# Performance work log

Measured on AMD Instinct MI355X. Metric: run time of the kernel, lower is better.

The kernel has to match this reference:

```python
import jax, jax.numpy as jnp
import numpy as np

N_NODES = 50000
N_EDGES = 640000
D_IN = 128
D_OUT = 128


def setup_inputs() -> dict:
    key = jax.random.key(0)
    k1, k2, k3, k4 = jax.random.split(key, 4)
    x = jax.random.normal(k1, (N_NODES, D_IN), dtype=jnp.float32)
    edge_index = jax.random.randint(k2, (2, N_EDGES), 0, N_NODES, dtype=jnp.int64)
    weight = jax.random.uniform(k3, (1,), dtype=jnp.float32)
    temperature = jnp.ones((1,), dtype=jnp.float32)
    W = jax.random.normal(k4, (D_IN, D_OUT), dtype=jnp.float32) * (1.0 / np.sqrt(D_IN))
    b = jnp.zeros((D_OUT,), dtype=jnp.float32)
    return {"x": x, "edge_index": edge_index, "weight": weight,
            "temperature": temperature, "W": W, "b": b}


def _gcn_conv(x, edge_index, W, b):
    N = x.shape[0]
    src, dst = edge_index[0], edge_index[1]
    loop = jnp.arange(N, dtype=edge_index.dtype)
    s = jnp.concatenate([src, loop])  # self-loops appended
    d = jnp.concatenate([dst, loop])
    deg = jax.ops.segment_sum(jnp.ones(s.shape[0], dtype=x.dtype), d, num_segments=N)
    dinv = jnp.where(deg > 0, deg ** -0.5, 0.0)
    norm = dinv[s] * dinv[d]  # [E+N]
    h = x @ W                 # linear transform first (PyG GCNConv)
    msg = h[s] * norm[:, None]
    out = jax.ops.segment_sum(msg, d, num_segments=N)
    return out + b


def _gradient_entropy(x, edge_index, temperature):
    # Boltzmann distribution over per-node Dirichlet energies;
    # entropy gradient w.r.t. node features (computed with autodiff).
    N = x.shape[0]
    src, dst = edge_index[0], edge_index[1]

    def entropy(z):
        diff = z[src] - z[dst]                                  # [E, D]
        E = jax.ops.segment_sum(jnp.sum(diff * diff, axis=-1), dst, num_segments=N)
        logp = jax.nn.log_softmax(-E / temperature[0])
        p = jnp.exp(logp)
        return -jnp.sum(p * logp)

    return jax.grad(entropy)(x)


def reference(x, edge_index, weight, temperature, W, b):
    h = _gcn_conv(x, edge_index, W, b)
    g = jax.lax.stop_gradient(_gradient_entropy(h, edge_index, temperature))
    return h + weight * g
```

## Files before the change

kernel.cpp:

```cpp
#include <hip/hip_runtime.h>

#define N_NODES 50000
#define N_EDGES 640000

#define OFF_HTMPB    0
#define OFF_OBF      3200000
#define OFF_DEG      6400000
#define OFF_ROWSTART 6450000
#define OFF_CURSOR   6500016
#define OFF_DINV     6550016
#define OFF_E        6600016
#define OFF_SCAL     6650016
#define OFF_BLKSUM   6650020
#define OFF_ESRC     6650276

typedef __attribute__((ext_vector_type(4))) short bf16x4;
typedef __attribute__((ext_vector_type(8))) short bf16x8;
typedef __attribute__((ext_vector_type(4))) float f32x4;

__device__ __forceinline__ unsigned short f2bf(float f) {
    unsigned u = __float_as_uint(f);
    unsigned r = u + 0x7fffu + ((u >> 16) & 1u);
    return (unsigned short)(r >> 16);
}
__device__ __forceinline__ float bflo(unsigned u) { return __uint_as_float(u << 16); }
__device__ __forceinline__ float bfhi(unsigned u) { return __uint_as_float(u & 0xffff0000u); }

__global__ __launch_bounds__(256) void k_init(float* ws) {
    int i = blockIdx.x * 256 + threadIdx.x;
    if (i < N_NODES) ((int*)(ws + OFF_DEG))[i] = 0;
    if (i == 0) {
        ((int*)(ws + OFF_SCAL))[0] = 0x7F7FFFFF;
        ws[OFF_SCAL + 1] = 0.f;
        ws[OFF_SCAL + 2] = 0.f;
    }
}

__global__ __launch_bounds__(256) void k_deg(const int* __restrict__ dst, int* __restrict__ deg) {
    int e = blockIdx.x * 256 + threadIdx.x;
    atomicAdd(&deg[dst[e]], 1);
}

__global__ __launch_bounds__(256) void k_gemm(const float* __restrict__ x,
                                              const float* __restrict__ W,
                                              unsigned short* __restrict__ htmpb) {
    __shared__ unsigned short xs[128 * 132];
    __shared__ unsigned short wt[128 * 132];
    int tid = threadIdx.x;
    int r0 = blockIdx.x * 128;

    #pragma unroll
    for (int i = 0; i < 16; i++) {
        int slot = tid + i * 256;
        int row = slot >> 5, c4 = slot & 31;
        float4 v = make_float4(0.f, 0.f, 0.f, 0.f);
        int gr = r0 + row;
        if (gr < N_NODES) v = *(const float4*)(x + gr * 128 + c4 * 4);
        uint2 pk;
        pk.x = (unsigned)f2bf(v.x) | ((unsigned)f2bf(v.y) << 16);
        pk.y = (unsigned)f2bf(v.z) | ((unsigned)f2bf(v.w) << 16);
        *(uint2*)(xs + row * 132 + c4 * 4) = pk;
    }
    #pragma unroll
    for (int i = 0; i < 16; i++) {
        int slot = tid + i * 256;
        int k = slot >> 5, n4 = (slot & 31) * 4;
        float4 v = *(const float4*)(W + k * 128 + n4);
        wt[(n4 + 0) * 132 + k] = f2bf(v.x);
        wt[(n4 + 1) * 132 + k] = f2bf(v.y);
        wt[(n4 + 2) * 132 + k] = f2bf(v.z);
        wt[(n4 + 3) * 132 + k] = f2bf(v.w);
    }
    __syncthreads();

    int wave = tid >> 6, lane = tid & 63;
    int quad = lane >> 4, m16 = lane & 15;
    f32x4 acc[2][8];
    #pragma unroll
    for (int r = 0; r < 2; r++)
        #pragma unroll
        for (int c = 0; c < 8; c++) acc[r][c] = (f32x4){0.f, 0.f, 0.f, 0.f};

    int arow = wave * 32 + m16;
    #pragma unroll
    for (int kt = 0; kt < 4; kt++) {
        int koff = kt * 32 + quad * 8;
        bf16x4 a0l = *(const bf16x4*)(xs + arow * 132 + koff);
        bf16x4 a0h = *(const bf16x4*)(xs + arow * 132 + koff + 4);
        bf16x4 a1l = *(const bf16x4*)(xs + (arow + 16) * 132 + koff);
        bf16x4 a1h = *(const bf16x4*)(xs + (arow + 16) * 132 + koff + 4);
        bf16x8 a0 = __builtin_shufflevector(a0l, a0h, 0, 1, 2, 3, 4, 5, 6, 7);
        bf16x8 a1 = __builtin_shufflevector(a1l, a1h, 0, 1, 2, 3, 4, 5, 6, 7);
        #pragma unroll
        for (int c = 0; c < 8; c++) {
            bf16x4 bl = *(const bf16x4*)(wt + (c * 16 + m16) * 132 + koff);
            bf16x4 bh = *(const bf16x4*)(wt + (c * 16 + m16) * 132 + koff + 4);
            bf16x8 bfrag = __builtin_shufflevector(bl, bh, 0, 1, 2, 3, 4, 5, 6, 7);
            acc[0][c] = __builtin_amdgcn_mfma_f32_16x16x32_bf16(a0, bfrag, acc[0][c], 0, 0, 0);
            acc[1][c] = __builtin_amdgcn_mfma_f32_16x16x32_bf16(a1, bfrag, acc[1][c], 0, 0, 0);
        }
    }
    #pragma unroll
    for (int r = 0; r < 2; r++) {
        #pragma unroll
        for (int reg = 0; reg < 4; reg++) {
            int grow = r0 + wave * 32 + r * 16 + quad * 4 + reg;
            if (grow < N_NODES) {
                #pragma unroll
                for (int c = 0; c < 8; c++)
                    htmpb[grow * 128 + c * 16 + m16] = f2bf(acc[r][c][reg]);
            }
        }
    }
}

__global__ __launch_bounds__(256) void k_scan1(const int* __restrict__ deg,
                                               int* __restrict__ rowstart,
                                               int* __restrict__ blksum,
                                               float* __restrict__ dinv) {
    __shared__ int sh[256];
    int i = blockIdx.x * 256 + threadIdx.x;
    int v = (i < N_NODES) ? deg[i] : 0;
    if (i < N_NODES) dinv[i] = rsqrtf((float)(v + 1));
    sh[threadIdx.x] = v;
    __syncthreads();
    #pragma unroll
    for (int off = 1; off < 256; off <<= 1) {
        int t = (threadIdx.x >= off) ? sh[threadIdx.x - off] : 0;
        __syncthreads();
        sh[threadIdx.x] += t;
        __syncthreads();
    }
    if (i < N_NODES) rowstart[i] = sh[threadIdx.x] - v;
    if (threadIdx.x == 255) blksum[blockIdx.x] = sh[255];
}

__global__ __launch_bounds__(256) void k_scan2(int* __restrict__ blksum, int nblk) {
    __shared__ int sh[256];
    int tid = threadIdx.x;
    int v = (tid < nblk) ? blksum[tid] : 0;
    sh[tid] = v;
    __syncthreads();
    #pragma unroll
    for (int off = 1; off < 256; off <<= 1) {
        int t = (tid >= off) ? sh[tid - off] : 0;
        __syncthreads();
        sh[tid] += t;
        __syncthreads();
    }
    if (tid < nblk) blksum[tid] = sh[tid] - v;
}

__global__ __launch_bounds__(256) void k_scan3(int* __restrict__ rowstart,
                                               const int* __restrict__ blksum,
                                               int* __restrict__ cursor) {
    int i = blockIdx.x * 256 + threadIdx.x;
    if (i < N_NODES) {
        rowstart[i] += blksum[blockIdx.x];
        cursor[i] = 0;
    }
    if (i == 0) rowstart[N_NODES] = N_EDGES;
}

__global__ __launch_bounds__(256) void k_bucket(const int* __restrict__ src,
                                                const int* __restrict__ dst,
                                                const int* __restrict__ rowstart,
                                                int* __restrict__ cursor,
                                                int* __restrict__ esrc) {
    int e = blockIdx.x * 256 + threadIdx.x;
    int d = dst[e];
    int pos = atomicAdd(&cursor[d], 1);
    esrc[rowstart[d] + pos] = src[e];
}

__global__ __launch_bounds__(256) void k_gather(const unsigned short* __restrict__ htmpb,
                                                const float* __restrict__ dinv,
                                                const float* __restrict__ b,
                                                const int* __restrict__ rowstart,
                                                const int* __restrict__ esrc,
                                                float* __restrict__ out,
                                                unsigned short* __restrict__ obf) {
    int node = blockIdx.x * 8 + (threadIdx.x >> 5);
    int lane = threadIdx.x & 31;
    float di = dinv[node];
    float4 bv = *(const float4*)(b + lane * 4);
    uint2 hv = *(const uint2*)(htmpb + node * 128 + lane * 4);
    float sl = di * di;
    float ax = bv.x + bflo(hv.x) * sl, ay = bv.y + bfhi(hv.x) * sl;
    float az = bv.z + bflo(hv.y) * sl, aw = bv.w + bfhi(hv.y) * sl;
    float cx = 0.f, cy = 0.f, cz = 0.f, cw = 0.f;
    int e0 = rowstart[node], e1 = rowstart[node + 1];
    int k = e0;
    for (; k + 1 < e1; k += 2) {
        int s0 = esrc[k], s1 = esrc[k + 1];
        float n0 = di * dinv[s0], n1 = di * dinv[s1];
        uint2 u0 = *(const uint2*)(htmpb + s0 * 128 + lane * 4);
        uint2 u1 = *(const uint2*)(htmpb + s1 * 128 + lane * 4);
        ax += bflo(u0.x) * n0; ay += bfhi(u0.x) * n0;
        az += bflo(u0.y) * n0; aw += bfhi(u0.y) * n0;
        cx += bflo(u1.x) * n1; cy += bfhi(u1.x) * n1;
        cz += bflo(u1.y) * n1; cw += bfhi(u1.y) * n1;
    }
    if (k < e1) {
        int s0 = esrc[k];
        float n0 = di * dinv[s0];
        uint2 u0 = *(const uint2*)(htmpb + s0 * 128 + lane * 4);
        ax += bflo(u0.x) * n0; ay += bfhi(u0.x) * n0;
        az += bflo(u0.y) * n0; aw += bfhi(u0.y) * n0;
    }
    ax += cx; ay += cy; az += cz; aw += cw;
    *(float4*)(out + node * 128 + lane * 4) = make_float4(ax, ay, az, aw);
    uint2 pk;
    pk.x = (unsigned)f2bf(ax) | ((unsigned)f2bf(ay) << 16);
    pk.y = (unsigned)f2bf(az) | ((unsigned)f2bf(aw) << 16);
    *(uint2*)(obf + node * 128 + lane * 4) = pk;
}

__global__ __launch_bounds__(256) void k_energy(const unsigned short* __restrict__ obf,
                                                const int* __restrict__ rowstart,
                                                const int* __restrict__ esrc,
                                                float* __restrict__ E) {
    int node = blockIdx.x * 8 + (threadIdx.x >> 5);
    int lane = threadIdx.x & 31;
    uint2 ud = *(const uint2*)(obf + node * 128 + lane * 4);
    float o0 = bflo(ud.x), o1 = bfhi(ud.x), o2 = bflo(ud.y), o3 = bfhi(ud.y);
    float acc = 0.f, acc2 = 0.f;
    int e0 = rowstart[node], e1 = rowstart[node + 1];
    int k = e0;
    for (; k + 1 < e1; k += 2) {
        int s0 = esrc[k], s1 = esrc[k + 1];
        uint2 a = *(const uint2*)(obf + s0 * 128 + lane * 4);
        uint2 c = *(const uint2*)(obf + s1 * 128 + lane * 4);
        float d0 = bflo(a.x) - o0, d1 = bfhi(a.x) - o1;
        float d2 = bflo(a.y) - o2, d3 = bfhi(a.y) - o3;
        float e4 = bflo(c.x) - o0, e5 = bfhi(c.x) - o1;
        float e6 = bflo(c.y) - o2, e7 = bfhi(c.y) - o3;
        acc  += d0 * d0 + d1 * d1 + d2 * d2 + d3 * d3;
        acc2 += e4 * e4 + e5 * e5 + e6 * e6 + e7 * e7;
    }
    if (k < e1) {
        int s0 = esrc[k];
        uint2 a = *(const uint2*)(obf + s0 * 128 + lane * 4);
        float d0 = bflo(a.x) - o0, d1 = bfhi(a.x) - o1;
        float d2 = bflo(a.y) - o2, d3 = bfhi(a.y) - o3;
        acc += d0 * d0 + d1 * d1 + d2 * d2 + d3 * d3;
    }
    acc += acc2;
    #pragma unroll
    for (int off = 16; off; off >>= 1) acc += __shfl_xor(acc, off);
    if (lane == 0) E[node] = acc;
}

__global__ __launch_bounds__(256) void k_emin(const float* __restrict__ E, int* __restrict__ scal) {
    __shared__ float sh[4];
    int i = blockIdx.x * 256 + threadIdx.x;
    float v = 3.402823466e38f;
    if (i < N_NODES) v = E[i];
    #pragma unroll
    for (int off = 32; off; off >>= 1) v = fminf(v, __shfl_xor(v, off));
    int lane = threadIdx.x & 63, wid = threadIdx.x >> 6;
    if (lane == 0) sh[wid] = v;
    __syncthreads();
    if (threadIdx.x == 0) {
        float m = fminf(fminf(sh[0], sh[1]), fminf(sh[2], sh[3]));
        atomicMin(scal, __float_as_int(m));
    }
}

__global__ __launch_bounds__(256) void k_sums(const float* __restrict__ E,
                                              const float* __restrict__ temp,
                                              const int* __restrict__ scal,
                                              float* __restrict__ S) {
    __shared__ float sh0[4], sh1[4];
    float Emin = __int_as_float(scal[0]);
    float T = temp[0];
    int i = blockIdx.x * 256 + threadIdx.x;
    float s0 = 0.f, s1 = 0.f;
    if (i < N_NODES) {
        float dd = (Emin - E[i]) / T;
        float ed = __expf(dd);
        s0 = ed; s1 = ed * dd;
    }
    #pragma unroll
    for (int off = 32; off; off >>= 1) { s0 += __shfl_xor(s0, off); s1 += __shfl_xor(s1, off); }
    int lane = threadIdx.x & 63, wid = threadIdx.x >> 6;
    if (lane == 0) { sh0[wid] = s0; sh1[wid] = s1; }
    __syncthreads();
    if (threadIdx.x == 0) {
        atomicAdd(&S[0], sh0[0] + sh0[1] + sh0[2] + sh0[3]);
        atomicAdd(&S[1], sh1[0] + sh1[1] + sh1[2] + sh1[3]);
    }
}

__global__ __launch_bounds__(256) void k_grad(const int* __restrict__ rowstart,
                                              const int* __restrict__ esrc,
                                              const float* __restrict__ E,
                                              const float* __restrict__ temp,
                                              const float* __restrict__ scal,
                                              const float* __restrict__ weight,
                                              float* __restrict__ out) {
    int node = blockIdx.x * 8 + (threadIdx.x >> 5);
    int lane = threadIdx.x & 31;
    float Emin = __int_as_float(((const int*)scal)[0]);
    float S0 = scal[1], S1 = scal[2];
    float T = temp[0];
    float dd = (Emin - E[node]) / T;
    float qd = (__expf(dd) / S0) * (dd - S1 / S0) / T;
    if (qd == 0.f) return;
    float cc = 2.f * weight[0] * qd;
    float4 od = *(const float4*)(out + node * 128 + lane * 4);
    float sx = 0.f, sy = 0.f, sz = 0.f, sw = 0.f;
    int e0 = rowstart[node], e1 = rowstart[node + 1];
    for (int k = e0; k < e1; k++) {
        int s = esrc[k];
        float4 a = *(const float4*)(out + s * 128 + lane * 4);
        float vx = cc * (a.x - od.x), vy = cc * (a.y - od.y);
        float vz = cc * (a.z - od.z), vw = cc * (a.w - od.w);
        float* os = out + s * 128 + lane * 4;
        atomicAdd(os + 0, vx); atomicAdd(os + 1, vy);
        atomicAdd(os + 2, vz); atomicAdd(os + 3, vw);
        sx += vx; sy += vy; sz += vz; sw += vw;
    }
    float* odp = out + node * 128 + lane * 4;
    atomicAdd(odp + 0, -sx); atomicAdd(odp + 1, -sy);
    atomicAdd(odp + 2, -sz); atomicAdd(odp + 3, -sw);
}

extern "C" void kernel_launch(void* const* d_in, const int* in_sizes, int n_in,
                              void* d_out, int out_size, void* d_ws, size_t ws_size,
                              hipStream_t stream) {
    const float* x      = (const float*)d_in[0];
    const int*   ei     = (const int*)d_in[1];
    const float* weight = (const float*)d_in[2];
    const float* temp   = (const float*)d_in[3];
    const float* W      = (const float*)d_in[4];
    const float* b      = (const float*)d_in[5];
    float* out = (float*)d_out;
    float* ws  = (float*)d_ws;

    const int* src = ei;
    const int* dst = ei + N_EDGES;

    unsigned short* htmpb = (unsigned short*)(ws + OFF_HTMPB);
    unsigned short* obf   = (unsigned short*)(ws + OFF_OBF);
    int*   deg      = (int*)(ws + OFF_DEG);
    int*   rowstart = (int*)(ws + OFF_ROWSTART);
    int*   cursor   = (int*)(ws + OFF_CURSOR);
    float* dinv     = ws + OFF_DINV;
    float* Earr     = ws + OFF_E;
    float* scal     = ws + OFF_SCAL;
    int*   blksum   = (int*)(ws + OFF_BLKSUM);
    int*   esrc     = (int*)(ws + OFF_ESRC);

    const int NBLK = 196;

    k_init<<<NBLK, 256, 0, stream>>>(ws);
    k_deg<<<N_EDGES / 256, 256, 0, stream>>>(dst, deg);
    k_gemm<<<391, 256, 0, stream>>>(x, W, htmpb);
    k_scan1<<<NBLK, 256, 0, stream>>>(deg, rowstart, blksum, dinv);
    k_scan2<<<1, 256, 0, stream>>>(blksum, NBLK);
    k_scan3<<<NBLK, 256, 0, stream>>>(rowstart, blksum, cursor);
    k_bucket<<<N_EDGES / 256, 256, 0, stream>>>(src, dst, rowstart, cursor, esrc);
    k_gather<<<6250, 256, 0, stream>>>(htmpb, dinv, b, rowstart, esrc, out, obf);
    k_energy<<<6250, 256, 0, stream>>>(obf, rowstart, esrc, Earr);
    k_emin<<<NBLK, 256, 0, stream>>>(Earr, (int*)scal);
    k_sums<<<NBLK, 256, 0, stream>>>(Earr, temp, (const int*)scal, scal + 1);
    k_grad<<<6250, 256, 0, stream>>>(rowstart, esrc, Earr, temp, scal, weight, out);
}
```

Baseline: 266.3 us.

## Fuse all stages into one persistent cooperative kernel with grid syncs

```diff
diff --git a/kernel.cpp b/kernel.cpp
--- a/kernel.cpp
+++ b/kernel.cpp
@@ -1,7 +1,11 @@
 #include <hip/hip_runtime.h>
+#include <hip/hip_cooperative_groups.h>
+
+namespace cg = cooperative_groups;
 
 #define N_NODES 50000
 #define N_EDGES 640000
+#define NSCANB  196
 
 #define OFF_HTMPB    0
 #define OFF_OBF      3200000
@@ -26,304 +30,272 @@
 __device__ __forceinline__ float bflo(unsigned u) { return __uint_as_float(u << 16); }
 __device__ __forceinline__ float bfhi(unsigned u) { return __uint_as_float(u & 0xffff0000u); }
 
-__global__ __launch_bounds__(256) void k_init(float* ws) {
-    int i = blockIdx.x * 256 + threadIdx.x;
-    if (i < N_NODES) ((int*)(ws + OFF_DEG))[i] = 0;
-    if (i == 0) {
-        ((int*)(ws + OFF_SCAL))[0] = 0x7F7FFFFF;
-        ws[OFF_SCAL + 1] = 0.f;
-        ws[OFF_SCAL + 2] = 0.f;
-    }
-}
-
-__global__ __launch_bounds__(256) void k_deg(const int* __restrict__ dst, int* __restrict__ deg) {
-    int e = blockIdx.x * 256 + threadIdx.x;
-    atomicAdd(&deg[dst[e]], 1);
-}
-
-__global__ __launch_bounds__(256) void k_gemm(const float* __restrict__ x,
-                                              const float* __restrict__ W,
-                                              unsigned short* __restrict__ htmpb) {
-    __shared__ unsigned short xs[128 * 132];
-    __shared__ unsigned short wt[128 * 132];
-    int tid = threadIdx.x;
-    int r0 = blockIdx.x * 128;
-
-    #pragma unroll
-    for (int i = 0; i < 16; i++) {
-        int slot = tid + i * 256;
-        int row = slot >> 5, c4 = slot & 31;
-        float4 v = make_float4(0.f, 0.f, 0.f, 0.f);
-        int gr = r0 + row;
-        if (gr < N_NODES) v = *(const float4*)(x + gr * 128 + c4 * 4);
-        uint2 pk;
-        pk.x = (unsigned)f2bf(v.x) | ((unsigned)f2bf(v.y) << 16);
-        pk.y = (unsigned)f2bf(v.z) | ((unsigned)f2bf(v.w) << 16);
-        *(uint2*)(xs + row * 132 + c4 * 4) = pk;
-    }
-    #pragma unroll
-    for (int i = 0; i < 16; i++) {
-        int slot = tid + i * 256;
-        int k = slot >> 5, n4 = (slot & 31) * 4;
-        float4 v = *(const float4*)(W + k * 128 + n4);
-        wt[(n4 + 0) * 132 + k] = f2bf(v.x);
-        wt[(n4 + 1) * 132 + k] = f2bf(v.y);
-        wt[(n4 + 2) * 132 + k] = f2bf(v.z);
-        wt[(n4 + 3) * 132 + k] = f2bf(v.w);
-    }
-    __syncthreads();
-
-    int wave = tid >> 6, lane = tid & 63;
-    int quad = lane >> 4, m16 = lane & 15;
-    f32x4 acc[2][8];
-    #pragma unroll
-    for (int r = 0; r < 2; r++)
+__global__ __launch_bounds__(256, 4) void k_fused(
+    const float* __restrict__ x, const int* __restrict__ ei,
+    const float* __restrict__ weight, const float* __restrict__ temp,
+    const float* __restrict__ W, const float* __restrict__ bias,
+    float* __restrict__ out, float* __restrict__ ws)
+{
+    cg::grid_group grid = cg::this_grid();
+    const int* src = ei;
+    const int* dst = ei + N_EDGES;
+    unsigned short* htmpb = (unsigned short*)(ws + OFF_HTMPB);
+    unsigned short* obf   = (unsigned short*)(ws + OFF_OBF);
+    int*   deg      = (int*)(ws + OFF_DEG);
+    int*   rowstart = (int*)(ws + OFF_ROWSTART);
+    int*   cursor   = (int*)(ws + OFF_CURSOR);
+    float* dinv     = ws + OFF_DINV;
+    float* E        = ws + OFF_E;
+    float* scal     = ws + OFF_SCAL;
+    int*   blksum   = (int*)(ws + OFF_BLKSUM);
+    int*   esrc     = (int*)(ws + OFF_ESRC);
+
+    const int tid  = threadIdx.x;
+    const int gtid = blockIdx.x * 256 + tid;
+    const int gsz  = gridDim.x * 256;
+
+    __shared__ union {
+        unsigned short wt[128 * 132];
+        int scan[256];
+    } u;
+    __shared__ int   ired[8];
+    __shared__ float fred[8];
+
+    for (int i = gtid; i < N_NODES; i += gsz) deg[i] = 0;
+    if (gtid == 0) { ((int*)scal)[0] = 0x7F7FFFFF; scal[1] = 0.f; scal[2] = 0.f; }
+    grid.sync();
+
+    for (int e = gtid; e < N_EDGES; e += gsz) atomicAdd(&deg[dst[e]], 1);
+
+    if (blockIdx.x < 782) {
+        for (int i = tid; i < 4096; i += 256) {
+            int k = i >> 5, n4 = (i & 31) * 4;
+            float4 v = *(const float4*)(W + k * 128 + n4);
+            u.wt[(n4 + 0) * 132 + k] = f2bf(v.x);
+            u.wt[(n4 + 1) * 132 + k] = f2bf(v.y);
+            u.wt[(n4 + 2) * 132 + k] = f2bf(v.z);
+            u.wt[(n4 + 3) * 132 + k] = f2bf(v.w);
+        }
+        __syncthreads();
+        int wave = tid >> 6, lane = tid & 63, quad = lane >> 4, m16 = lane & 15;
+        for (int t = blockIdx.x; t < 782; t += gridDim.x) {
+            int r0 = t * 64;
+            int arow = r0 + wave * 16 + m16;
+            int rowc = arow < N_NODES ? arow : N_NODES - 1;
+            f32x4 acc[8];
+            #pragma unroll
+            for (int c = 0; c < 8; c++) acc[c] = (f32x4){0.f, 0.f, 0.f, 0.f};
+            #pragma unroll
+            for (int kt = 0; kt < 4; kt++) {
+                int koff = kt * 32 + quad * 8;
+                float4 xa = *(const float4*)(x + rowc * 128 + koff);
+                float4 xb = *(const float4*)(x + rowc * 128 + koff + 4);
+                bf16x8 af;
+                af[0] = (short)f2bf(xa.x); af[1] = (short)f2bf(xa.y);
+                af[2] = (short)f2bf(xa.z); af[3] = (short)f2bf(xa.w);
+                af[4] = (short)f2bf(xb.x); af[5] = (short)f2bf(xb.y);
+                af[6] = (short)f2bf(xb.z); af[7] = (short)f2bf(xb.w);
+                #pragma unroll
+                for (int c = 0; c < 8; c++) {
+                    bf16x4 bl = *(const bf16x4*)(u.wt + (c * 16 + m16) * 132 + koff);
+                    bf16x4 bh = *(const bf16x4*)(u.wt + (c * 16 + m16) * 132 + koff + 4);
+                    bf16x8 bfrag = __builtin_shufflevector(bl, bh, 0, 1, 2, 3, 4, 5, 6, 7);
+                    acc[c] = __builtin_amdgcn_mfma_f32_16x16x32_bf16(af, bfrag, acc[c], 0, 0, 0);
+                }
+            }
+            #pragma unroll
+            for (int reg = 0; reg < 4; reg++) {
+                int grow = r0 + wave * 16 + quad * 4 + reg;
+                if (grow < N_NODES) {
+                    #pragma unroll
+                    for (int c = 0; c < 8; c++)
+                        htmpb[grow * 128 + c * 16 + m16] = f2bf(acc[c][reg]);
+                }
+            }
+        }
+    }
+    grid.sync();
+
+    for (int vb = blockIdx.x; vb < NSCANB; vb += gridDim.x) {
+        int i = vb * 256 + tid;
+        int v = (i < N_NODES) ? deg[i] : 0;
+        if (i < N_NODES) dinv[i] = rsqrtf((float)(v + 1));
+        u.scan[tid] = v;
+        __syncthreads();
         #pragma unroll
-        for (int c = 0; c < 8; c++) acc[r][c] = (f32x4){0.f, 0.f, 0.f, 0.f};
-
-    int arow = wave * 32 + m16;
-    #pragma unroll
-    for (int kt = 0; kt < 4; kt++) {
-        int koff = kt * 32 + quad * 8;
-        bf16x4 a0l = *(const bf16x4*)(xs + arow * 132 + koff);
-        bf16x4 a0h = *(const bf16x4*)(xs + arow * 132 + koff + 4);
-        bf16x4 a1l = *(const bf16x4*)(xs + (arow + 16) * 132 + koff);
-        bf16x4 a1h = *(const bf16x4*)(xs + (arow + 16) * 132 + koff + 4);
-        bf16x8 a0 = __builtin_shufflevector(a0l, a0h, 0, 1, 2, 3, 4, 5, 6, 7);
-        bf16x8 a1 = __builtin_shufflevector(a1l, a1h, 0, 1, 2, 3, 4, 5, 6, 7);
+        for (int off = 1; off < 256; off <<= 1) {
+            int t2 = (tid >= off) ? u.scan[tid - off] : 0;
+            __syncthreads();
+            u.scan[tid] += t2;
+            __syncthreads();
+        }
+        if (i < N_NODES) rowstart[i] = u.scan[tid] - v;
+        if (tid == 255) blksum[vb] = u.scan[255];
+        __syncthreads();
+    }
+    grid.sync();
+
+    for (int vb = blockIdx.x; vb < NSCANB; vb += gridDim.x) {
+        int lane = tid & 63, wid = tid >> 6;
+        int p = (tid < vb) ? blksum[tid] : 0;
         #pragma unroll
-        for (int c = 0; c < 8; c++) {
-            bf16x4 bl = *(const bf16x4*)(wt + (c * 16 + m16) * 132 + koff);
-            bf16x4 bh = *(const bf16x4*)(wt + (c * 16 + m16) * 132 + koff + 4);
-            bf16x8 bfrag = __builtin_shufflevector(bl, bh, 0, 1, 2, 3, 4, 5, 6, 7);
-            acc[0][c] = __builtin_amdgcn_mfma_f32_16x16x32_bf16(a0, bfrag, acc[0][c], 0, 0, 0);
-            acc[1][c] = __builtin_amdgcn_mfma_f32_16x16x32_bf16(a1, bfrag, acc[1][c], 0, 0, 0);
-        }
-    }
-    #pragma unroll
-    for (int r = 0; r < 2; r++) {
+        for (int off = 32; off; off >>= 1) p += __shfl_xor(p, off);
+        if (lane == 0) ired[wid] = p;
+        __syncthreads();
+        int offp = ired[0] + ired[1] + ired[2] + ired[3];
+        int i = vb * 256 + tid;
+        if (i < N_NODES) { rowstart[i] += offp; cursor[i] = 0; }
+        __syncthreads();
+    }
+    if (gtid == 0) rowstart[N_NODES] = N_EDGES;
+    grid.sync();
+
+    for (int e = gtid; e < N_EDGES; e += gsz) {
+        int d = dst[e];
+        int pos = atomicAdd(&cursor[d], 1);
+        esrc[rowstart[d] + pos] = src[e];
+    }
+    grid.sync();
+
+    {
+        int lane = tid & 31;
+        for (int node = blockIdx.x * 8 + (tid >> 5); node < N_NODES; node += gridDim.x * 8) {
+            float di = dinv[node];
+            float4 bv = *(const float4*)(bias + lane * 4);
+            uint2 hv = *(const uint2*)(htmpb + node * 128 + lane * 4);
+            float sl = di * di;
+            float ax = bv.x + bflo(hv.x) * sl, ay = bv.y + bfhi(hv.x) * sl;
+            float az = bv.z + bflo(hv.y) * sl, aw = bv.w + bfhi(hv.y) * sl;
+            float cx = 0.f, cy = 0.f, cz = 0.f, cw = 0.f;
+            int e0 = rowstart[node], e1 = rowstart[node + 1];
+            int k = e0;
+            for (; k + 1 < e1; k += 2) {
+                int s0 = esrc[k], s1 = esrc[k + 1];
+                float n0 = di * dinv[s0], n1 = di * dinv[s1];
+                uint2 u0 = *(const uint2*)(htmpb + s0 * 128 + lane * 4);
+                uint2 u1 = *(const uint2*)(htmpb + s1 * 128 + lane * 4);
+                ax += bflo(u0.x) * n0; ay += bfhi(u0.x) * n0;
+                az += bflo(u0.y) * n0; aw += bfhi(u0.y) * n0;
+                cx += bflo(u1.x) * n1; cy += bfhi(u1.x) * n1;
+                cz += bflo(u1.y) * n1; cw += bfhi(u1.y) * n1;
+            }
+            if (k < e1) {
+                int s0 = esrc[k];
+                float n0 = di * dinv[s0];
+                uint2 u0 = *(const uint2*)(htmpb + s0 * 128 + lane * 4);
+                ax += bflo(u0.x) * n0; ay += bfhi(u0.x) * n0;
+                az += bflo(u0.y) * n0; aw += bfhi(u0.y) * n0;
+            }
+            ax += cx; ay += cy; az += cz; aw += cw;
+            *(float4*)(out + node * 128 + lane * 4) = make_float4(ax, ay, az, aw);
+            uint2 pk;
+            pk.x = (unsigned)f2bf(ax) | ((unsigned)f2bf(ay) << 16);
+            pk.y = (unsigned)f2bf(az) | ((unsigned)f2bf(aw) << 16);
+            *(uint2*)(obf + node * 128 + lane * 4) = pk;
+        }
+    }
+    grid.sync();
+
+    {
+        int lane = tid & 31;
+        for (int node = blockIdx.x * 8 + (tid >> 5); node < N_NODES; node += gridDim.x * 8) {
+            uint2 ud = *(const uint2*)(obf + node * 128 + lane * 4);
+            float o0 = bflo(ud.x), o1 = bfhi(ud.x), o2 = bflo(ud.y), o3 = bfhi(ud.y);
+            float acc = 0.f, acc2 = 0.f;
+            int e0 = rowstart[node], e1 = rowstart[node + 1];
+            int k = e0;
+            for (; k + 1 < e1; k += 2) {
+                int s0 = esrc[k], s1 = esrc[k + 1];
+                uint2 a = *(const uint2*)(obf + s0 * 128 + lane * 4);
+                uint2 c = *(const uint2*)(obf + s1 * 128 + lane * 4);
+                float d0 = bflo(a.x) - o0, d1 = bfhi(a.x) - o1;
+                float d2 = bflo(a.y) - o2, d3 = bfhi(a.y) - o3;
+                float e4 = bflo(c.x) - o0, e5 = bfhi(c.x) - o1;
+                float e6 = bflo(c.y) - o2, e7 = bfhi(c.y) - o3;
+                acc  += d0 * d0 + d1 * d1 + d2 * d2 + d3 * d3;
+                acc2 += e4 * e4 + e5 * e5 + e6 * e6 + e7 * e7;
+            }
+            if (k < e1) {
+                int s0 = esrc[k];
+                uint2 a = *(const uint2*)(obf + s0 * 128 + lane * 4);
+                float d0 = bflo(a.x) - o0, d1 = bfhi(a.x) - o1;
+                float d2 = bflo(a.y) - o2, d3 = bfhi(a.y) - o3;
+                acc += d0 * d0 + d1 * d1 + d2 * d2 + d3 * d3;
+            }
+            acc += acc2;
+            #pragma unroll
+            for (int off = 16; off; off >>= 1) acc += __shfl_xor(acc, off);
+            if (lane == 0) E[node] = acc;
+        }
+    }
+    grid.sync();
+
+    {
+        float v = 3.402823466e38f;
+        for (int i = gtid; i < N_NODES; i += gsz) v = fminf(v, E[i]);
+        int lane = tid & 63, wid = tid >> 6;
         #pragma unroll
-        for (int reg = 0; reg < 4; reg++) {
-            int grow = r0 + wave * 32 + r * 16 + quad * 4 + reg;
-            if (grow < N_NODES) {
-                #pragma unroll
-                for (int c = 0; c < 8; c++)
-                    htmpb[grow * 128 + c * 16 + m16] = f2bf(acc[r][c][reg]);
-            }
-        }
-    }
-}
-
-__global__ __launch_bounds__(256) void k_scan1(const int* __restrict__ deg,
-                                               int* __restrict__ rowstart,
-                                               int* __restrict__ blksum,
-                                               float* __restrict__ dinv) {
-    __shared__ int sh[256];
-    int i = blockIdx.x * 256 + threadIdx.x;
-    int v = (i < N_NODES) ? deg[i] : 0;
-    if (i < N_NODES) dinv[i] = rsqrtf((float)(v + 1));
-    sh[threadIdx.x] = v;
-    __syncthreads();
-    #pragma unroll
-    for (int off = 1; off < 256; off <<= 1) {
-        int t = (threadIdx.x >= off) ? sh[threadIdx.x - off] : 0;
-        __syncthreads();
-        sh[threadIdx.x] += t;
-        __syncthreads();
-    }
-    if (i < N_NODES) rowstart[i] = sh[threadIdx.x] - v;
-    if (threadIdx.x == 255) blksum[blockIdx.x] = sh[255];
-}
-
-__global__ __launch_bounds__(256) void k_scan2(int* __restrict__ blksum, int nblk) {
-    __shared__ int sh[256];
-    int tid = threadIdx.x;
-    int v = (tid < nblk) ? blksum[tid] : 0;
-    sh[tid] = v;
-    __syncthreads();
-    #pragma unroll
-    for (int off = 1; off < 256; off <<= 1) {
-        int t = (tid >= off) ? sh[tid - off] : 0;
-        __syncthreads();
-        sh[tid] += t;
-        __syncthreads();
-    }
-    if (tid < nblk) blksum[tid] = sh[tid] - v;
-}
-
-__global__ __launch_bounds__(256) void k_scan3(int* __restrict__ rowstart,
-                                               const int* __restrict__ blksum,
-                                               int* __restrict__ cursor) {
-    int i = blockIdx.x * 256 + threadIdx.x;
-    if (i < N_NODES) {
-        rowstart[i] += blksum[blockIdx.x];
-        cursor[i] = 0;
-    }
-    if (i == 0) rowstart[N_NODES] = N_EDGES;
-}
-
-__global__ __launch_bounds__(256) void k_bucket(const int* __restrict__ src,
-                                                const int* __restrict__ dst,
-                                                const int* __restrict__ rowstart,
-                                                int* __restrict__ cursor,
-                                                int* __restrict__ esrc) {
-    int e = blockIdx.x * 256 + threadIdx.x;
-    int d = dst[e];
-    int pos = atomicAdd(&cursor[d], 1);
-    esrc[rowstart[d] + pos] = src[e];
-}
-
-__global__ __launch_bounds__(256) void k_gather(const unsigned short* __restrict__ htmpb,
-                                                const float* __restrict__ dinv,
-                                                const float* __restrict__ b,
-                                                const int* __restrict__ rowstart,
-                                                const int* __restrict__ esrc,
-                                                float* __restrict__ out,
-                                                unsigned short* __restrict__ obf) {
-    int node = blockIdx.x * 8 + (threadIdx.x >> 5);
-    int lane = threadIdx.x & 31;
-    float di = dinv[node];
-    float4 bv = *(const float4*)(b + lane * 4);
-    uint2 hv = *(const uint2*)(htmpb + node * 128 + lane * 4);
-    float sl = di * di;
-    float ax = bv.x + bflo(hv.x) * sl, ay = bv.y + bfhi(hv.x) * sl;
-    float az = bv.z + bflo(hv.y) * sl, aw = bv.w + bfhi(hv.y) * sl;
-    float cx = 0.f, cy = 0.f, cz = 0.f, cw = 0.f;
-    int e0 = rowstart[node], e1 = rowstart[node + 1];
-    int k = e0;
-    for (; k + 1 < e1; k += 2) {
-        int s0 = esrc[k], s1 = esrc[k + 1];
-        float n0 = di * dinv[s0], n1 = di * dinv[s1];
-        uint2 u0 = *(const uint2*)(htmpb + s0 * 128 + lane * 4);
-        uint2 u1 = *(const uint2*)(htmpb + s1 * 128 + lane * 4);
-        ax += bflo(u0.x) * n0; ay += bfhi(u0.x) * n0;
-        az += bflo(u0.y) * n0; aw += bfhi(u0.y) * n0;
-        cx += bflo(u1.x) * n1; cy += bfhi(u1.x) * n1;
-        cz += bflo(u1.y) * n1; cw += bfhi(u1.y) * n1;
-    }
-    if (k < e1) {
-        int s0 = esrc[k];
-        float n0 = di * dinv[s0];
-        uint2 u0 = *(const uint2*)(htmpb + s0 * 128 + lane * 4);
-        ax += bflo(u0.x) * n0; ay += bfhi(u0.x) * n0;
-        az += bflo(u0.y) * n0; aw += bfhi(u0.y) * n0;
-    }
-    ax += cx; ay += cy; az += cz; aw += cw;
-    *(float4*)(out + node * 128 + lane * 4) = make_float4(ax, ay, az, aw);
-    uint2 pk;
-    pk.x = (unsigned)f2bf(ax) | ((unsigned)f2bf(ay) << 16);
-    pk.y = (unsigned)f2bf(az) | ((unsigned)f2bf(aw) << 16);
-    *(uint2*)(obf + node * 128 + lane * 4) = pk;
-}
-
-__global__ __launch_bounds__(256) void k_energy(const unsigned short* __restrict__ obf,
-                                                const int* __restrict__ rowstart,
-                                                const int* __restrict__ esrc,
-                                                float* __restrict__ E) {
-    int node = blockIdx.x * 8 + (threadIdx.x >> 5);
-    int lane = threadIdx.x & 31;
-    uint2 ud = *(const uint2*)(obf + node * 128 + lane * 4);
-    float o0 = bflo(ud.x), o1 = bfhi(ud.x), o2 = bflo(ud.y), o3 = bfhi(ud.y);
-    float acc = 0.f, acc2 = 0.f;
-    int e0 = rowstart[node], e1 = rowstart[node + 1];
-    int k = e0;
-    for (; k + 1 < e1; k += 2) {
-        int s0 = esrc[k], s1 = esrc[k + 1];
-        uint2 a = *(const uint2*)(obf + s0 * 128 + lane * 4);
-        uint2 c = *(const uint2*)(obf + s1 * 128 + lane * 4);
-        float d0 = bflo(a.x) - o0, d1 = bfhi(a.x) - o1;
-        float d2 = bflo(a.y) - o2, d3 = bfhi(a.y) - o3;
-        float e4 = bflo(c.x) - o0, e5 = bfhi(c.x) - o1;
-        float e6 = bflo(c.y) - o2, e7 = bfhi(c.y) - o3;
-        acc  += d0 * d0 + d1 * d1 + d2 * d2 + d3 * d3;
-        acc2 += e4 * e4 + e5 * e5 + e6 * e6 + e7 * e7;
-    }
-    if (k < e1) {
-        int s0 = esrc[k];
-        uint2 a = *(const uint2*)(obf + s0 * 128 + lane * 4);
-        float d0 = bflo(a.x) - o0, d1 = bfhi(a.x) - o1;
-        float d2 = bflo(a.y) - o2, d3 = bfhi(a.y) - o3;
-        acc += d0 * d0 + d1 * d1 + d2 * d2 + d3 * d3;
-    }
-    acc += acc2;
-    #pragma unroll
-    for (int off = 16; off; off >>= 1) acc += __shfl_xor(acc, off);
-    if (lane == 0) E[node] = acc;
-}
-
-__global__ __launch_bounds__(256) void k_emin(const float* __restrict__ E, int* __restrict__ scal) {
-    __shared__ float sh[4];
-    int i = blockIdx.x * 256 + threadIdx.x;
-    float v = 3.402823466e38f;
-    if (i < N_NODES) v = E[i];
-    #pragma unroll
-    for (int off = 32; off; off >>= 1) v = fminf(v, __shfl_xor(v, off));
-    int lane = threadIdx.x & 63, wid = threadIdx.x >> 6;
-    if (lane == 0) sh[wid] = v;
-    __syncthreads();
-    if (threadIdx.x == 0) {
-        float m = fminf(fminf(sh[0], sh[1]), fminf(sh[2], sh[3]));
-        atomicMin(scal, __float_as_int(m));
-    }
-}
-
-__global__ __launch_bounds__(256) void k_sums(const float* __restrict__ E,
-                                              const float* __restrict__ temp,
-                                              const int* __restrict__ scal,
-                                              float* __restrict__ S) {
-    __shared__ float sh0[4], sh1[4];
-    float Emin = __int_as_float(scal[0]);
-    float T = temp[0];
-    int i = blockIdx.x * 256 + threadIdx.x;
-    float s0 = 0.f, s1 = 0.f;
-    if (i < N_NODES) {
-        float dd = (Emin - E[i]) / T;
-        float ed = __expf(dd);
-        s0 = ed; s1 = ed * dd;
-    }
-    #pragma unroll
-    for (int off = 32; off; off >>= 1) { s0 += __shfl_xor(s0, off); s1 += __shfl_xor(s1, off); }
-    int lane = threadIdx.x & 63, wid = threadIdx.x >> 6;
-    if (lane == 0) { sh0[wid] = s0; sh1[wid] = s1; }
-    __syncthreads();
-    if (threadIdx.x == 0) {
-        atomicAdd(&S[0], sh0[0] + sh0[1] + sh0[2] + sh0[3]);
-        atomicAdd(&S[1], sh1[0] + sh1[1] + sh1[2] + sh1[3]);
-    }
-}
-
-__global__ __launch_bounds__(256) void k_grad(const int* __restrict__ rowstart,
-                                              const int* __restrict__ esrc,
-                                              const float* __restrict__ E,
-                                              const float* __restrict__ temp,
-                                              const float* __restrict__ scal,
-                                              const float* __restrict__ weight,
-                                              float* __restrict__ out) {
-    int node = blockIdx.x * 8 + (threadIdx.x >> 5);
-    int lane = threadIdx.x & 31;
-    float Emin = __int_as_float(((const int*)scal)[0]);
-    float S0 = scal[1], S1 = scal[2];
-    float T = temp[0];
-    float dd = (Emin - E[node]) / T;
-    float qd = (__expf(dd) / S0) * (dd - S1 / S0) / T;
-    if (qd == 0.f) return;
-    float cc = 2.f * weight[0] * qd;
-    float4 od = *(const float4*)(out + node * 128 + lane * 4);
-    float sx = 0.f, sy = 0.f, sz = 0.f, sw = 0.f;
-    int e0 = rowstart[node], e1 = rowstart[node + 1];
-    for (int k = e0; k < e1; k++) {
-        int s = esrc[k];
-        float4 a = *(const float4*)(out + s * 128 + lane * 4);
-        float vx = cc * (a.x - od.x), vy = cc * (a.y - od.y);
-        float vz = cc * (a.z - od.z), vw = cc * (a.w - od.w);
-        float* os = out + s * 128 + lane * 4;
-        atomicAdd(os + 0, vx); atomicAdd(os + 1, vy);
-        atomicAdd(os + 2, vz); atomicAdd(os + 3, vw);
-        sx += vx; sy += vy; sz += vz; sw += vw;
-    }
-    float* odp = out + node * 128 + lane * 4;
-    atomicAdd(odp + 0, -sx); atomicAdd(odp + 1, -sy);
-    atomicAdd(odp + 2, -sz); atomicAdd(odp + 3, -sw);
+        for (int off = 32; off; off >>= 1) v = fminf(v, __shfl_xor(v, off));
+        if (lane == 0) fred[wid] = v;
+        __syncthreads();
+        if (tid == 0) {
+            float m = fminf(fminf(fred[0], fred[1]), fminf(fred[2], fred[3]));
+            atomicMin((int*)scal, __float_as_int(m));
+        }
+    }
+    grid.sync();
+
+    {
+        float Emin = __int_as_float(((int*)scal)[0]);
+        float T = temp[0];
+        float s0 = 0.f, s1 = 0.f;
+        for (int i = gtid; i < N_NODES; i += gsz) {
+            float dd = (Emin - E[i]) / T;
+            float ed = __expf(dd);
+            s0 += ed; s1 += ed * dd;
+        }
+        int lane = tid & 63, wid = tid >> 6;
+        #pragma unroll
+        for (int off = 32; off; off >>= 1) { s0 += __shfl_xor(s0, off); s1 += __shfl_xor(s1, off); }
+        if (lane == 0) { fred[wid] = s0; fred[wid + 4] = s1; }
+        __syncthreads();
+        if (tid == 0) {
+            atomicAdd(&scal[1], fred[0] + fred[1] + fred[2] + fred[3]);
+            atomicAdd(&scal[2], fred[4] + fred[5] + fred[6] + fred[7]);
+        }
+    }
+    grid.sync();
+
+    {
+        float Emin = __int_as_float(((int*)scal)[0]);
+        float S0 = scal[1], S1 = scal[2];
+        float T = temp[0];
+        float wscale = 2.f * weight[0];
+        int lane = tid & 31;
+        for (int node = blockIdx.x * 8 + (tid >> 5); node < N_NODES; node += gridDim.x * 8) {
+            float dd = (Emin - E[node]) / T;
+            float qd = (__expf(dd) / S0) * (dd - S1 / S0) / T;
+            if (qd != 0.f) {
+                float cc = wscale * qd;
+                float4 od = *(const float4*)(out + node * 128 + lane * 4);
+                float sx = 0.f, sy = 0.f, sz = 0.f, sw = 0.f;
+                int e0 = rowstart[node], e1 = rowstart[node + 1];
+                for (int k = e0; k < e1; k++) {
+                    int s = esrc[k];
+                    float4 a = *(const float4*)(out + s * 128 + lane * 4);
+                    float vx = cc * (a.x - od.x), vy = cc * (a.y - od.y);
+                    float vz = cc * (a.z - od.z), vw = cc * (a.w - od.w);
+                    float* os = out + s * 128 + lane * 4;
+                    atomicAdd(os + 0, vx); atomicAdd(os + 1, vy);
+                    atomicAdd(os + 2, vz); atomicAdd(os + 3, vw);
+                    sx += vx; sy += vy; sz += vz; sw += vw;
+                }
+                float* odp = out + node * 128 + lane * 4;
+                atomicAdd(odp + 0, -sx); atomicAdd(odp + 1, -sy);
+                atomicAdd(odp + 2, -sz); atomicAdd(odp + 3, -sw);
+            }
+        }
+    }
 }
 
 extern "C" void kernel_launch(void* const* d_in, const int* in_sizes, int n_in,
@@ -334,36 +306,20 @@
     const float* weight = (const float*)d_in[2];
     const float* temp   = (const float*)d_in[3];
     const float* W      = (const float*)d_in[4];
-    const float* b      = (const float*)d_in[5];
+    const float* bias   = (const float*)d_in[5];
     float* out = (float*)d_out;
     float* ws  = (float*)d_ws;
 
-    const int* src = ei;
-    const int* dst = ei + N_EDGES;
-
-    unsigned short* htmpb = (unsigned short*)(ws + OFF_HTMPB);
-    unsigned short* obf   = (unsigned short*)(ws + OFF_OBF);
-    int*   deg      = (int*)(ws + OFF_DEG);
-    int*   rowstart = (int*)(ws + OFF_ROWSTART);
-    int*   cursor   = (int*)(ws + OFF_CURSOR);
-    float* dinv     = ws + OFF_DINV;
-    float* Earr     = ws + OFF_E;
-    float* scal     = ws + OFF_SCAL;
-    int*   blksum   = (int*)(ws + OFF_BLKSUM);
-    int*   esrc     = (int*)(ws + OFF_ESRC);
-
-    const int NBLK = 196;
-
-    k_init<<<NBLK, 256, 0, stream>>>(ws);
-    k_deg<<<N_EDGES / 256, 256, 0, stream>>>(dst, deg);
-    k_gemm<<<391, 256, 0, stream>>>(x, W, htmpb);
-    k_scan1<<<NBLK, 256, 0, stream>>>(deg, rowstart, blksum, dinv);
-    k_scan2<<<1, 256, 0, stream>>>(blksum, NBLK);
-    k_scan3<<<NBLK, 256, 0, stream>>>(rowstart, blksum, cursor);
-    k_bucket<<<N_EDGES / 256, 256, 0, stream>>>(src, dst, rowstart, cursor, esrc);
-    k_gather<<<6250, 256, 0, stream>>>(htmpb, dinv, b, rowstart, esrc, out, obf);
-    k_energy<<<6250, 256, 0, stream>>>(obf, rowstart, esrc, Earr);
-    k_emin<<<NBLK, 256, 0, stream>>>(Earr, (int*)scal);
-    k_sums<<<NBLK, 256, 0, stream>>>(Earr, temp, (const int*)scal, scal + 1);
-    k_grad<<<6250, 256, 0, stream>>>(rowstart, esrc, Earr, temp, scal, weight, out);
+    int maxB = 0;
+    if (hipOccupancyMaxActiveBlocksPerMultiprocessor(&maxB, k_fused, 256, 0) != hipSuccess || maxB <= 0)
+        maxB = 2;
+    int grid = maxB * 256;
+    if (grid > 2048) grid = 2048;
+
+    void* args[8];
+    args[0] = (void*)&x;     args[1] = (void*)&ei;
+    args[2] = (void*)&weight; args[3] = (void*)&temp;
+    args[4] = (void*)&W;     args[5] = (void*)&bias;
+    args[6] = (void*)&out;   args[7] = (void*)&ws;
+    hipLaunchCooperativeKernel((const void*)k_fused, dim3(grid), dim3(256), args, 0, stream);
 }
```

Result: slower. 867.5 us (+225.7%).

## Fuse degree count into GEMM, merge scan passes, fold min into energy

Applied to the files above, without the earlier changes.

```diff
diff --git a/kernel.cpp b/kernel.cpp
--- a/kernel.cpp
+++ b/kernel.cpp
@@ -2,6 +2,7 @@
 
 #define N_NODES 50000
 #define N_EDGES 640000
+#define NSCANB  196
 
 #define OFF_HTMPB    0
 #define OFF_OBF      3200000
@@ -36,35 +37,18 @@
     }
 }
 
-__global__ __launch_bounds__(256) void k_deg(const int* __restrict__ dst, int* __restrict__ deg) {
-    int e = blockIdx.x * 256 + threadIdx.x;
-    atomicAdd(&deg[dst[e]], 1);
-}
-
-__global__ __launch_bounds__(256) void k_gemm(const float* __restrict__ x,
-                                              const float* __restrict__ W,
-                                              unsigned short* __restrict__ htmpb) {
-    __shared__ unsigned short xs[128 * 132];
+__global__ __launch_bounds__(256) void k_deg_gemm(const float* __restrict__ x,
+                                                  const int* __restrict__ dst,
+                                                  const float* __restrict__ W,
+                                                  int* __restrict__ deg,
+                                                  unsigned short* __restrict__ htmpb) {
+    int gtid = blockIdx.x * 256 + threadIdx.x;
+    for (int e = gtid; e < N_EDGES; e += 782 * 256) atomicAdd(&deg[dst[e]], 1);
+
     __shared__ unsigned short wt[128 * 132];
     int tid = threadIdx.x;
-    int r0 = blockIdx.x * 128;
-
-    #pragma unroll
-    for (int i = 0; i < 16; i++) {
-        int slot = tid + i * 256;
-        int row = slot >> 5, c4 = slot & 31;
-        float4 v = make_float4(0.f, 0.f, 0.f, 0.f);
-        int gr = r0 + row;
-        if (gr < N_NODES) v = *(const float4*)(x + gr * 128 + c4 * 4);
-        uint2 pk;
-        pk.x = (unsigned)f2bf(v.x) | ((unsigned)f2bf(v.y) << 16);
-        pk.y = (unsigned)f2bf(v.z) | ((unsigned)f2bf(v.w) << 16);
-        *(uint2*)(xs + row * 132 + c4 * 4) = pk;
-    }
-    #pragma unroll
-    for (int i = 0; i < 16; i++) {
-        int slot = tid + i * 256;
-        int k = slot >> 5, n4 = (slot & 31) * 4;
+    for (int i = tid; i < 4096; i += 256) {
+        int k = i >> 5, n4 = (i & 31) * 4;
         float4 v = *(const float4*)(W + k * 128 + n4);
         wt[(n4 + 0) * 132 + k] = f2bf(v.x);
         wt[(n4 + 1) * 132 + k] = f2bf(v.y);
@@ -73,43 +57,38 @@
     }
     __syncthreads();
 
-    int wave = tid >> 6, lane = tid & 63;
-    int quad = lane >> 4, m16 = lane & 15;
-    f32x4 acc[2][8];
-    #pragma unroll
-    for (int r = 0; r < 2; r++)
-        #pragma unroll
-        for (int c = 0; c < 8; c++) acc[r][c] = (f32x4){0.f, 0.f, 0.f, 0.f};
-
-    int arow = wave * 32 + m16;
+    int wave = tid >> 6, lane = tid & 63, quad = lane >> 4, m16 = lane & 15;
+    int r0 = blockIdx.x * 64;
+    int arow = r0 + wave * 16 + m16;
+    int rowc = arow < N_NODES ? arow : N_NODES - 1;
+    f32x4 acc[8];
+    #pragma unroll
+    for (int c = 0; c < 8; c++) acc[c] = (f32x4){0.f, 0.f, 0.f, 0.f};
     #pragma unroll
     for (int kt = 0; kt < 4; kt++) {
         int koff = kt * 32 + quad * 8;
-        bf16x4 a0l = *(const bf16x4*)(xs + arow * 132 + koff);
-        bf16x4 a0h = *(const bf16x4*)(xs + arow * 132 + koff + 4);
-        bf16x4 a1l = *(const bf16x4*)(xs + (arow + 16) * 132 + koff);
-        bf16x4 a1h = *(const bf16x4*)(xs + (arow + 16) * 132 + koff + 4);
-        bf16x8 a0 = __builtin_shufflevector(a0l, a0h, 0, 1, 2, 3, 4, 5, 6, 7);
-        bf16x8 a1 = __builtin_shufflevector(a1l, a1h, 0, 1, 2, 3, 4, 5, 6, 7);
+        float4 xa = *(const float4*)(x + rowc * 128 + koff);
+        float4 xb = *(const float4*)(x + rowc * 128 + koff + 4);
+        bf16x8 af;
+        af[0] = (short)f2bf(xa.x); af[1] = (short)f2bf(xa.y);
+        af[2] = (short)f2bf(xa.z); af[3] = (short)f2bf(xa.w);
+        af[4] = (short)f2bf(xb.x); af[5] = (short)f2bf(xb.y);
+        af[6] = (short)f2bf(xb.z); af[7] = (short)f2bf(xb.w);
         #pragma unroll
         for (int c = 0; c < 8; c++) {
             bf16x4 bl = *(const bf16x4*)(wt + (c * 16 + m16) * 132 + koff);
             bf16x4 bh = *(const bf16x4*)(wt + (c * 16 + m16) * 132 + koff + 4);
             bf16x8 bfrag = __builtin_shufflevector(bl, bh, 0, 1, 2, 3, 4, 5, 6, 7);
-            acc[0][c] = __builtin_amdgcn_mfma_f32_16x16x32_bf16(a0, bfrag, acc[0][c], 0, 0, 0);
-            acc[1][c] = __builtin_amdgcn_mfma_f32_16x16x32_bf16(a1, bfrag, acc[1][c], 0, 0, 0);
+            acc[c] = __builtin_amdgcn_mfma_f32_16x16x32_bf16(af, bfrag, acc[c], 0, 0, 0);
         }
     }
     #pragma unroll
-    for (int r = 0; r < 2; r++) {
-        #pragma unroll
-        for (int reg = 0; reg < 4; reg++) {
-            int grow = r0 + wave * 32 + r * 16 + quad * 4 + reg;
-            if (grow < N_NODES) {
-                #pragma unroll
-                for (int c = 0; c < 8; c++)
-                    htmpb[grow * 128 + c * 16 + m16] = f2bf(acc[r][c][reg]);
-            }
+    for (int reg = 0; reg < 4; reg++) {
+        int grow = r0 + wave * 16 + quad * 4 + reg;
+        if (grow < N_NODES) {
+            #pragma unroll
+            for (int c = 0; c < 8; c++)
+                htmpb[grow * 128 + c * 16 + m16] = f2bf(acc[c][reg]);
         }
     }
 }
@@ -135,31 +114,21 @@
     if (threadIdx.x == 255) blksum[blockIdx.x] = sh[255];
 }
 
-__global__ __launch_bounds__(256) void k_scan2(int* __restrict__ blksum, int nblk) {
-    __shared__ int sh[256];
-    int tid = threadIdx.x;
-    int v = (tid < nblk) ? blksum[tid] : 0;
-    sh[tid] = v;
-    __syncthreads();
-    #pragma unroll
-    for (int off = 1; off < 256; off <<= 1) {
-        int t = (tid >= off) ? sh[tid - off] : 0;
-        __syncthreads();
-        sh[tid] += t;
-        __syncthreads();
-    }
-    if (tid < nblk) blksum[tid] = sh[tid] - v;
-}
-
-__global__ __launch_bounds__(256) void k_scan3(int* __restrict__ rowstart,
-                                               const int* __restrict__ blksum,
-                                               int* __restrict__ cursor) {
-    int i = blockIdx.x * 256 + threadIdx.x;
-    if (i < N_NODES) {
-        rowstart[i] += blksum[blockIdx.x];
-        cursor[i] = 0;
-    }
-    if (i == 0) rowstart[N_NODES] = N_EDGES;
+__global__ __launch_bounds__(256) void k_scan23(int* __restrict__ rowstart,
+                                                const int* __restrict__ blksum,
+                                                int* __restrict__ cursor) {
+    __shared__ int ired[4];
+    int vb = blockIdx.x, tid = threadIdx.x;
+    int lane = tid & 63, wid = tid >> 6;
+    int p = (tid < vb) ? blksum[tid] : 0;
+    #pragma unroll
+    for (int off = 32; off; off >>= 1) p += __shfl_xor(p, off);
+    if (lane == 0) ired[wid] = p;
+    __syncthreads();
+    int offp = ired[0] + ired[1] + ired[2] + ired[3];
+    int i = vb * 256 + tid;
+    if (i < N_NODES) { rowstart[i] += offp; cursor[i] = 0; }
+    if (vb == 0 && tid == 0) rowstart[N_NODES] = N_EDGES;
 }
 
 __global__ __launch_bounds__(256) void k_bucket(const int* __restrict__ src,
@@ -219,7 +188,9 @@
 __global__ __launch_bounds__(256) void k_energy(const unsigned short* __restrict__ obf,
                                                 const int* __restrict__ rowstart,
                                                 const int* __restrict__ esrc,
-                                                float* __restrict__ E) {
+                                                float* __restrict__ E,
+                                                int* __restrict__ scal) {
+    __shared__ float smin[8];
     int node = blockIdx.x * 8 + (threadIdx.x >> 5);
     int lane = threadIdx.x & 31;
     uint2 ud = *(const uint2*)(obf + node * 128 + lane * 4);
@@ -248,21 +219,12 @@
     acc += acc2;
     #pragma unroll
     for (int off = 16; off; off >>= 1) acc += __shfl_xor(acc, off);
-    if (lane == 0) E[node] = acc;
-}
-
-__global__ __launch_bounds__(256) void k_emin(const float* __restrict__ E, int* __restrict__ scal) {
-    __shared__ float sh[4];
-    int i = blockIdx.x * 256 + threadIdx.x;
-    float v = 3.402823466e38f;
-    if (i < N_NODES) v = E[i];
-    #pragma unroll
-    for (int off = 32; off; off >>= 1) v = fminf(v, __shfl_xor(v, off));
-    int lane = threadIdx.x & 63, wid = threadIdx.x >> 6;
-    if (lane == 0) sh[wid] = v;
+    if (lane == 0) { E[node] = acc; smin[threadIdx.x >> 5] = acc; }
     __syncthreads();
     if (threadIdx.x == 0) {
-        float m = fminf(fminf(sh[0], sh[1]), fminf(sh[2], sh[3]));
+        float m = smin[0];
+        #pragma unroll
+        for (int g = 1; g < 8; g++) m = fminf(m, smin[g]);
         atomicMin(scal, __float_as_int(m));
     }
 }
@@ -352,18 +314,13 @@
     int*   blksum   = (int*)(ws + OFF_BLKSUM);
     int*   esrc     = (int*)(ws + OFF_ESRC);
 
-    const int NBLK = 196;
-
-    k_init<<<NBLK, 256, 0, stream>>>(ws);
-    k_deg<<<N_EDGES / 256, 256, 0, stream>>>(dst, deg);
-    k_gemm<<<391, 256, 0, stream>>>(x, W, htmpb);
-    k_scan1<<<NBLK, 256, 0, stream>>>(deg, rowstart, blksum, dinv);
-    k_scan2<<<1, 256, 0, stream>>>(blksum, NBLK);
-    k_scan3<<<NBLK, 256, 0, stream>>>(rowstart, blksum, cursor);
+    k_init<<<NSCANB, 256, 0, stream>>>(ws);
+    k_deg_gemm<<<782, 256, 0, stream>>>(x, dst, W, deg, htmpb);
+    k_scan1<<<NSCANB, 256, 0, stream>>>(deg, rowstart, blksum, dinv);
+    k_scan23<<<NSCANB, 256, 0, stream>>>(rowstart, blksum, cursor);
     k_bucket<<<N_EDGES / 256, 256, 0, stream>>>(src, dst, rowstart, cursor, esrc);
     k_gather<<<6250, 256, 0, stream>>>(htmpb, dinv, b, rowstart, esrc, out, obf);
-    k_energy<<<6250, 256, 0, stream>>>(obf, rowstart, esrc, Earr);
-    k_emin<<<NBLK, 256, 0, stream>>>(Earr, (int*)scal);
-    k_sums<<<NBLK, 256, 0, stream>>>(Earr, temp, (const int*)scal, scal + 1);
+    k_energy<<<6250, 256, 0, stream>>>(obf, rowstart, esrc, Earr, (int*)scal);
+    k_sums<<<NSCANB, 256, 0, stream>>>(Earr, temp, (const int*)scal, scal + 1);
     k_grad<<<6250, 256, 0, stream>>>(rowstart, esrc, Earr, temp, scal, weight, out);
 }
```

New measurement: 308.8 us. 1.16x slower.
